# Optimization experiments

Hardware: AMD Instinct MI355X
Metric: run time of the kernel (lower is better)

## Reference

```python
import jax, jax.numpy as jnp
import numpy as np

N, E, G = 50000, 500000, 2048
IN_ATOM, IN_BOND, H, OUT = 128, 16, 256, 2


def setup_inputs() -> dict:
    key = jax.random.key(0)
    ks = iter(jax.random.split(key, 64))
    nrm = lambda shape, s=0.05: jax.random.normal(next(ks), shape, dtype=jnp.float32) * s
    inp = {}
    inp["x"] = nrm((N, IN_ATOM), 1.0)
    inp["edge_attr"] = nrm((E, IN_BOND), 1.0)
    inp["edge_index"] = jax.random.randint(next(ks), (2, E), 0, N)
    inp["batch"] = jnp.sort(jax.random.randint(next(ks), (N,), 0, G))
    dims = [IN_ATOM, H, H]  # input width of each GINE layer
    for i, d in enumerate(dims):
        inp[f"l{i}_We"] = nrm((IN_BOND, d))            # GINEConv edge lin
        inp[f"l{i}_be"] = jnp.zeros((d,), jnp.float32)
        inp[f"l{i}_W1"] = nrm((d, H))                  # mlp Linear 1
        inp[f"l{i}_b1"] = jnp.zeros((H,), jnp.float32)
        inp[f"l{i}_W2"] = nrm((H, H))                  # mlp Linear 2
        inp[f"l{i}_b2"] = jnp.zeros((H,), jnp.float32)
        inp[f"l{i}_eps"] = jnp.zeros((1,), jnp.float32)  # train_eps scalar
    # Bayesian head: weight = mu + exp(log_sigma) * noise
    inp["h1_wmu"] = nrm((H, H)); inp["h1_wls"] = jnp.full((H, H), -3.0, jnp.float32)
    inp["h1_bmu"] = jnp.zeros((H,), jnp.float32); inp["h1_bls"] = jnp.full((H,), -3.0, jnp.float32)
    inp["h2_wmu"] = nrm((H, OUT)); inp["h2_wls"] = jnp.full((H, OUT), -3.0, jnp.float32)
    inp["h2_bmu"] = jnp.zeros((OUT,), jnp.float32); inp["h2_bls"] = jnp.full((OUT,), -3.0, jnp.float32)
    inp["eps_w1"] = nrm((H, H), 1.0); inp["eps_b1"] = nrm((H,), 1.0)
    inp["eps_w2"] = nrm((H, OUT), 1.0); inp["eps_b2"] = nrm((OUT,), 1.0)
    return inp


def _gine_layer(h, src, dst, edge_attr, We, be, W1, b1, W2, b2, eps):
    e = edge_attr @ We + be                       # [E, d] edge projection
    m = jax.nn.relu(h[src] + e)                   # messages from source nodes
    agg = jax.ops.segment_sum(m, dst, num_segments=N)
    z = (1.0 + eps[0]) * h + agg
    z = jax.nn.relu(z @ W1 + b1) @ W2 + b2        # GINE mlp
    return jax.nn.relu(z)                          # backbone activation


def reference(x, edge_attr,
              l0_We, l0_be, l0_W1, l0_b1, l0_W2, l0_b2, l0_eps,
              l1_We, l1_be, l1_W1, l1_b1, l1_W2, l1_b2, l1_eps,
              l2_We, l2_be, l2_W1, l2_b1, l2_W2, l2_b2, l2_eps,
              h1_wmu, h1_wls, h1_bmu, h1_bls,
              h2_wmu, h2_wls, h2_bmu, h2_bls,
              eps_w1, eps_b1, eps_w2, eps_b2,
              edge_index, batch):
    src, dst = edge_index[0], edge_index[1]
    h = x
    layers = [
        (l0_We, l0_be, l0_W1, l0_b1, l0_W2, l0_b2, l0_eps),
        (l1_We, l1_be, l1_W1, l1_b1, l1_W2, l1_b2, l1_eps),
        (l2_We, l2_be, l2_W1, l2_b1, l2_W2, l2_b2, l2_eps),
    ]
    for (We, be, W1, b1, W2, b2, eps) in layers:
        h = _gine_layer(h, src, dst, edge_attr, We, be, W1, b1, W2, b2, eps)
    hg = jax.ops.segment_sum(h, batch, num_segments=G)  # global_add_pool -> [G, H]
    # Bayesian head (dropout is identity at eval)
    w1 = h1_wmu + jnp.exp(h1_wls) * eps_w1
    b1 = h1_bmu + jnp.exp(h1_bls) * eps_b1
    h1 = jax.nn.silu(hg @ w1 + b1)
    w2 = h2_wmu + jnp.exp(h2_wls) * eps_w2
    b2 = h2_bmu + jnp.exp(h2_bls) * eps_b2
    return h1 @ w2 + b2  # [G, OUT]
```

## Files before the change

### kernel.cpp

```cpp
#include <hip/hip_runtime.h>
#include <hip/hip_bf16.h>
#include <math.h>


#define THREADS 256

typedef __attribute__((ext_vector_type(8))) short bf16x8;
typedef __attribute__((ext_vector_type(4))) float f32x4;

__device__ __forceinline__ unsigned short f2bf(float x) {
    __hip_bfloat16 h = __float2bfloat16(x);
    return __builtin_bit_cast(unsigned short, h);
}
__device__ __forceinline__ float bflo(unsigned u) {
    return __builtin_bit_cast(float, u << 16);
}
__device__ __forceinline__ float bfhi(unsigned u) {
    return __builtin_bit_cast(float, u & 0xffff0000u);
}
__device__ __forceinline__ float bf2f(unsigned short u) {
    return __builtin_bit_cast(float, (unsigned)u << 16);
}
__device__ __forceinline__ unsigned pk(float a, float b) {
    return (unsigned)f2bf(a) | ((unsigned)f2bf(b) << 16);
}

__global__ __launch_bounds__(THREADS) void hist_kernel(
    const int* __restrict__ ei, int* __restrict__ deg, int E)
{
    int e = blockIdx.x * THREADS + threadIdx.x;
    if (e < E) atomicAdd(&deg[ei[E + e]], 1);
}

__global__ __launch_bounds__(1024) void scan_kernel(
    int* __restrict__ deg, int* __restrict__ rowptr, int n)
{
    __shared__ int wsum[16];
    __shared__ int carry_s;
    const int t    = threadIdx.x;
    const int lane = t & 63, wv = t >> 6;
    if (t == 0) carry_s = 0;
    __syncthreads();
    for (int base = 0; base < n; base += 4096) {
        int i = base + t * 4;
        int4 v = make_int4(0, 0, 0, 0);
        if (i + 3 < n) {
            v = *(const int4*)(deg + i);
            *(int4*)(deg + i) = make_int4(0, 0, 0, 0);
        } else if (i < n) {
            v.x = deg[i];                    deg[i] = 0;
            if (i + 1 < n) { v.y = deg[i+1]; deg[i+1] = 0; }
            if (i + 2 < n) { v.z = deg[i+2]; deg[i+2] = 0; }
        }
        int p1 = v.x + v.y, p2 = p1 + v.z, tot = p2 + v.w;
        int incl = tot;
#pragma unroll
        for (int off = 1; off < 64; off <<= 1) {
            int u = __shfl_up(incl, off, 64);
            if (lane >= off) incl += u;
        }
        if (lane == 63) wsum[wv] = incl;
        __syncthreads();
        if (wv == 0) {
            int s = (lane < 16) ? wsum[lane] : 0;
#pragma unroll
            for (int off = 1; off < 16; off <<= 1) {
                int u = __shfl_up(s, off, 64);
                if (lane >= off) s += u;
            }
            if (lane < 16) wsum[lane] = s;
        }
        __syncthreads();
        int waveoff = (wv == 0) ? 0 : wsum[wv - 1];
        int tbase   = carry_s + waveoff + incl - tot;
        if (i     < n) rowptr[i + 1] = tbase + v.x;
        if (i + 1 < n) rowptr[i + 2] = tbase + p1;
        if (i + 2 < n) rowptr[i + 3] = tbase + p2;
        if (i + 3 < n) rowptr[i + 4] = tbase + tot;
        __syncthreads();
        if (t == 1023) carry_s = carry_s + wsum[15];
        __syncthreads();
    }
    if (t == 0) rowptr[0] = 0;
}

__global__ __launch_bounds__(THREADS) void fill_kernel(
    const int* __restrict__ ei, const int* __restrict__ rowptr,
    int* __restrict__ cursor, int* __restrict__ csr_src,
    int* __restrict__ csr_dst, const float* __restrict__ edge_attr,
    unsigned short* __restrict__ ea16, int E)
{
    int e = blockIdx.x * THREADS + threadIdx.x;
    if (e >= E) return;
    int s = ei[e], d = ei[E + e];
    int pos  = atomicAdd(&cursor[d], 1);
    int slot = rowptr[d] + pos;
    csr_src[slot] = s;
    csr_dst[slot] = d;
    const float4* a = (const float4*)(edge_attr + (size_t)e * 16);
    float4 a0 = a[0], a1 = a[1], a2 = a[2], a3 = a[3];
    uint4* dst = (uint4*)(ea16 + (size_t)slot * 16);
    dst[0] = make_uint4(pk(a0.x, a0.y), pk(a0.z, a0.w), pk(a1.x, a1.y), pk(a1.z, a1.w));
    dst[1] = make_uint4(pk(a2.x, a2.y), pk(a2.z, a2.w), pk(a3.x, a3.y), pk(a3.z, a3.w));
}

__global__ __launch_bounds__(THREADS) void xprep_kernel(
    const float* __restrict__ x, unsigned short* __restrict__ xbf, int n4,
    uint4* __restrict__ aggz, int nAgg4,
    float4* __restrict__ hgz, int nHg4)
{
    int i = blockIdx.x * THREADS + threadIdx.x;
    if (i < n4) {
        float4 v = ((const float4*)x)[i];
        uint2 p;
        p.x = pk(v.x, v.y);
        p.y = pk(v.z, v.w);
        ((uint2*)xbf)[i] = p;
    }
    if (i < nAgg4) aggz[i] = make_uint4(0, 0, 0, 0);
    if (i < nHg4)  hgz[i]  = make_float4(0.f, 0.f, 0.f, 0.f);
}

struct PrepArgs {
    const float* W[6]; unsigned short* Wt[6]; int K[6];
    const float* mu; const float* ls; const float* eps; float* w1buf;
    const float* We[3]; unsigned short* Wp[3]; int D[3];
};
__global__ __launch_bounds__(THREADS) void prep_kernel(PrepArgs a)
{
    __shared__ float tile[32][33];
    const int z = blockIdx.z;
    const int t = threadIdx.x;

    if (z < 6) {
        const int K = a.K[z];
        const int kb = blockIdx.x * 32;
        if (kb >= K) return;
        const float* W = a.W[z];
        unsigned short* Wt = a.Wt[z];
        const int nb = blockIdx.y * 32;
        const int tx = t & 31, ty = t >> 5;
#pragma unroll
        for (int i = ty; i < 32; i += 8)
            tile[i][tx] = W[(size_t)(kb + i) * 256 + nb + tx];
        __syncthreads();
#pragma unroll
        for (int i = ty; i < 32; i += 8)
            Wt[(size_t)(nb + i) * K + kb + tx] = f2bf(tile[tx][i]);
    } else if (z == 6) {
        int blk = blockIdx.x + blockIdx.y * 8;
#pragma unroll
        for (int c = 0; c < 4; c++) {
            int i = blk * THREADS + t + c * 16384;
            a.w1buf[i] = a.mu[i] + expf(a.ls[i]) * a.eps[i];
        }
    } else {
        int l = blockIdx.x + blockIdx.y * 8;
        if (l >= 3) return;
        int D = a.D[l];
        if (t >= D) return;
        const float* We = a.We[l];
        unsigned short* Wp = a.Wp[l];
#pragma unroll
        for (int k = 0; k < 16; k++) Wp[t * 32 + k] = f2bf(We[k * D + t]);
#pragma unroll
        for (int k = 16; k < 32; k++) Wp[t * 32 + k] = 0;
    }
}

template<int D>
__global__ __launch_bounds__(THREADS) void edge_agg_kernel(
    const unsigned short* __restrict__ hbf,
    const unsigned short* __restrict__ ea16,
    const int* __restrict__ csr_src,
    const int* __restrict__ csr_dst,
    const unsigned short* __restrict__ Wtp,
    const float* __restrict__ be,
    unsigned short* __restrict__ agg,
    int E)
{
    constexpr int EPB = (D == 128) ? 64 : 32;
    constexpr int LDF = D + 8;
    __shared__ unsigned short msg[EPB * LDF];
    __shared__ int src_s[EPB];
    __shared__ int dst_x[EPB + 2];

    const int t    = threadIdx.x;
    const int e0   = blockIdx.x * EPB;
    const int lane = t & 63, wid = t >> 6;
    const int l15  = lane & 15, lgr = lane >> 4;

    for (int i = t; i < EPB; i += THREADS) {
        int e = e0 + i;
        src_s[i] = (e < E) ? csr_src[e] : 0;
    }
    for (int i = t; i < EPB + 2; i += THREADS) {
        int e = e0 + i - 1;
        dst_x[i] = (e < 0) ? -2 : ((e < E) ? csr_dst[e] : -1);
    }

    const int fb = (D == 128) ? (wid & 1) * 64 : wid * 64;
    const int eb = (D == 128) ? (wid >> 1) * 32 : 0;

    bf16x8 af[4];
#pragma unroll
    for (int mf = 0; mf < 4; mf++)
        af[mf] = *(const bf16x8*)(Wtp + (unsigned)(fb + mf * 16 + l15) * 32 + lgr * 8);

    f32x4 acc[4][2];
#pragma unroll
    for (int mf = 0; mf < 4; mf++) {
        int fpos = fb + mf * 16 + lgr * 4;
        float4 bv4 = *(const float4*)(be + fpos);
        f32x4 binit = (f32x4){bv4.x, bv4.y, bv4.z, bv4.w};
        acc[mf][0] = binit;
        acc[mf][1] = binit;
    }

#pragma unroll
    for (int nf = 0; nf < 2; nf++) {
        int er = e0 + eb + nf * 16 + l15;
        bf16x8 bv = (bf16x8){0, 0, 0, 0, 0, 0, 0, 0};
        if (lgr < 2 && er < E)
            bv = *(const bf16x8*)(ea16 + (size_t)er * 16 + lgr * 8);
#pragma unroll
        for (int mf = 0; mf < 4; mf++)
            acc[mf][nf] = __builtin_amdgcn_mfma_f32_16x16x32_bf16(
                af[mf], bv, acc[mf][nf], 0, 0, 0);
    }

#pragma unroll
    for (int nf = 0; nf < 2; nf++) {
        int edge = eb + nf * 16 + l15;
#pragma unroll
        for (int mf = 0; mf < 4; mf++) {
            int fpos = fb + mf * 16 + lgr * 4;
            f32x4 v = acc[mf][nf];
            uint2 p;
            p.x = pk(v[0], v[1]);
            p.y = pk(v[2], v[3]);
            *(uint2*)(&msg[edge * LDF + fpos]) = p;
        }
    }
    __syncthreads();

    constexpr int LPF = D / 2;
    const int f2   = (t & (LPF - 1)) * 2;
    const int win  = t / LPF;
    const int base = win * 16;

    unsigned hv[16], pv[16];
#pragma unroll
    for (int i = 0; i < 16; i++) {
        unsigned off = (unsigned)src_s[base + i] * D + f2;
        hv[i] = *(const unsigned*)(hbf + off);
        pv[i] = *(const unsigned*)(&msg[(base + i) * LDF + f2]);
    }

    float a0 = 0.f, a1 = 0.f;
    int  cur = dst_x[base + 1];
    bool rs  = (dst_x[base] != cur);

#pragma unroll
    for (int i = 0; i < 16; ++i) {
        int el = base + i;
        int d  = dst_x[el + 1];
        if (d != cur) {
            if (cur >= 0) {
                unsigned short* ap = agg + ((unsigned)cur * D + f2);
                unsigned v32 = pk(a0, a1);
                if (rs) {
                    *(unsigned*)ap = v32;
                } else {
                    asm volatile("global_atomic_pk_add_bf16 %0, %1, off"
                                 :: "v"(ap), "v"(v32) : "memory");
                }
            }
            a0 = 0.f; a1 = 0.f; rs = true; cur = d;
        }
        a0 += fmaxf(bflo(hv[i]) + bflo(pv[i]), 0.f);
        a1 += fmaxf(bfhi(hv[i]) + bfhi(pv[i]), 0.f);
    }
    if (cur >= 0) {
        bool re = (dst_x[base + 17] != cur);
        unsigned short* ap = agg + ((unsigned)cur * D + f2);
        unsigned v32 = pk(a0, a1);
        if (rs && re) {
            *(unsigned*)ap = v32;
        } else {
            asm volatile("global_atomic_pk_add_bf16 %0, %1, off"
                         :: "v"(ap), "v"(v32) : "memory");
        }
    }
}

template<int KIN, bool ZERO>
__global__ __launch_bounds__(THREADS) void fused_mlp_kernel(
    const unsigned short* __restrict__ hin,
    const unsigned short* __restrict__ agg,
    const unsigned short* __restrict__ Wt1,
    const float* __restrict__ b1,
    const unsigned short* __restrict__ Wt2,
    const float* __restrict__ b2,
    const float* __restrict__ epsp,
    unsigned short* __restrict__ out,
    uint4* __restrict__ aggz,
    int nrows)
{
    constexpr int LDT = 264;
    __shared__ short Buf[64 * LDT];

    const int t    = threadIdx.x;
    const int lane = t & 63;
    const int wid  = t >> 6;
    const int l15  = lane & 15, lgr = lane >> 4;
    const int r0   = blockIdx.x * 64;

    const float scale = 1.0f + epsp[0];

    constexpr int RU = KIN / 8;
#pragma unroll
    for (int c = 0; c < (64 * RU) / THREADS; c++) {
        int idx = t + c * THREADS;
        int r   = idx / RU;
        int kq  = idx % RU;
        int row = r0 + r;
        uint4 o = make_uint4(0, 0, 0, 0);
        if (row < nrows) {
            size_t g = (size_t)row * KIN + kq * 8;
            uint4 hv = *(const uint4*)(hin + g);
            uint4 av = *(const uint4*)(agg + g);
            o.x = pk(scale * bflo(hv.x) + bflo(av.x),
                     scale * bfhi(hv.x) + bfhi(av.x));
            o.y = pk(scale * bflo(hv.y) + bflo(av.y),
                     scale * bfhi(hv.y) + bfhi(av.y));
            o.z = pk(scale * bflo(hv.z) + bflo(av.z),
                     scale * bfhi(hv.z) + bfhi(av.z));
            o.w = pk(scale * bflo(hv.w) + bflo(av.w),
                     scale * bfhi(hv.w) + bfhi(av.w));
        }
        *(uint4*)(&Buf[r * LDT + kq * 8]) = o;
    }
    __syncthreads();

    if (ZERO) {
        const unsigned aggTot8 = (unsigned)nrows * 32;
        const uint4 zz = make_uint4(0, 0, 0, 0);
        if (KIN == 256) {
            unsigned b8 = (unsigned)blockIdx.x * 2048;
#pragma unroll
            for (int c = 0; c < 8; c++) {
                unsigned idx = b8 + t + c * THREADS;
                if (idx < aggTot8) aggz[idx] = zz;
            }
        } else {
            unsigned own  = (unsigned)blockIdx.x * 1024;
            unsigned tail = ((unsigned)gridDim.x + (unsigned)blockIdx.x) * 1024;
#pragma unroll
            for (int c = 0; c < 4; c++) {
                unsigned i1 = own + t + c * THREADS;
                if (i1 < aggTot8) aggz[i1] = zz;
                unsigned i2 = tail + t + c * THREADS;
                if (i2 < aggTot8) aggz[i2] = zz;
            }
        }
    }

    f32x4 acc[4][4];
#pragma unroll
    for (int nf = 0; nf < 4; nf++) {
        float bv = b1[wid * 64 + nf * 16 + l15];
#pragma unroll
        for (int mf = 0; mf < 4; mf++)
            acc[mf][nf] = (f32x4){bv, bv, bv, bv};
    }

#pragma unroll
    for (int k0 = 0; k0 < KIN; k0 += 64) {
#pragma unroll
        for (int ks = 0; ks < 2; ks++) {
            bf16x8 afr[4], bfr[4];
#pragma unroll
            for (int nf = 0; nf < 4; nf++)
                bfr[nf] = *(const bf16x8*)(Wt1 +
                    (size_t)(wid * 64 + nf * 16 + l15) * KIN + k0 + ks * 32 + lgr * 8);
#pragma unroll
            for (int mf = 0; mf < 4; mf++)
                afr[mf] = *(const bf16x8*)(&Buf[(mf * 16 + l15) * LDT + k0 + ks * 32 + lgr * 8]);
#pragma unroll
            for (int mf = 0; mf < 4; mf++)
#pragma unroll
                for (int nf = 0; nf < 4; nf++)
                    acc[mf][nf] = __builtin_amdgcn_mfma_f32_16x16x32_bf16(
                        afr[mf], bfr[nf], acc[mf][nf], 0, 0, 0);
        }
    }
    __syncthreads();

#pragma unroll
    for (int nf = 0; nf < 4; nf++) {
        int col = wid * 64 + nf * 16 + l15;
#pragma unroll
        for (int mf = 0; mf < 4; mf++) {
            f32x4 v = acc[mf][nf];
#pragma unroll
            for (int r = 0; r < 4; r++) {
                int row = mf * 16 + lgr * 4 + r;
                Buf[row * LDT + col] = (short)f2bf(fmaxf(v[r], 0.f));
            }
        }
    }
#pragma unroll
    for (int nf = 0; nf < 4; nf++) {
        float bv = b2[wid * 64 + nf * 16 + l15];
#pragma unroll
        for (int mf = 0; mf < 4; mf++)
            acc[mf][nf] = (f32x4){bv, bv, bv, bv};
    }
    __syncthreads();

#pragma unroll
    for (int k0 = 0; k0 < 256; k0 += 64) {
#pragma unroll
        for (int ks = 0; ks < 2; ks++) {
            bf16x8 afr[4], bfr[4];
#pragma unroll
            for (int nf = 0; nf < 4; nf++)
                bfr[nf] = *(const bf16x8*)(Wt2 +
                    (size_t)(wid * 64 + nf * 16 + l15) * 256 + k0 + ks * 32 + lgr * 8);
#pragma unroll
            for (int mf = 0; mf < 4; mf++)
                afr[mf] = *(const bf16x8*)(&Buf[(mf * 16 + l15) * LDT + k0 + ks * 32 + lgr * 8]);
#pragma unroll
            for (int mf = 0; mf < 4; mf++)
#pragma unroll
                for (int nf = 0; nf < 4; nf++)
                    acc[mf][nf] = __builtin_amdgcn_mfma_f32_16x16x32_bf16(
                        afr[mf], bfr[nf], acc[mf][nf], 0, 0, 0);
        }
    }

#pragma unroll
    for (int nf = 0; nf < 4; nf++) {
        int col = wid * 64 + nf * 16 + l15;
#pragma unroll
        for (int mf = 0; mf < 4; mf++) {
            f32x4 v = acc[mf][nf];
#pragma unroll
            for (int r = 0; r < 4; r++) {
                int row = r0 + mf * 16 + lgr * 4 + r;
                if (row < nrows)
                    out[(size_t)row * 256 + col] = f2bf(fmaxf(v[r], 0.f));
            }
        }
    }
}

__global__ __launch_bounds__(THREADS) void pool_kernel(
    const unsigned short* __restrict__ hbf,
    const int*   __restrict__ batch,
    float*       __restrict__ hg,
    int nnodes)
{
    constexpr int CH = 64;
    __shared__ int b_s[CH];
    const int t  = threadIdx.x;
    const int v0 = blockIdx.x * CH;
    int cnt = nnodes - v0;
    if (cnt > CH) cnt = CH;
    if (cnt <= 0) return;
    if (t < cnt) b_s[t] = batch[v0 + t];
    __syncthreads();

    int curb  = b_s[0];
    float acc = 0.f;
    for (int v = 0; v < cnt; v++) {
        int b = b_s[v];
        if (b != curb) {
            atomicAdd(&hg[(size_t)curb * 256 + t], acc);
            acc = 0.f; curb = b;
        }
        acc += bf2f(hbf[(size_t)(v0 + v) * 256 + t]);
    }
    atomicAdd(&hg[(size_t)curb * 256 + t], acc);
}

__global__ __launch_bounds__(THREADS) void head_kernel(
    const float* __restrict__ hg,
    const float* __restrict__ w1,
    const float* __restrict__ h1_bmu, const float* __restrict__ h1_bls,
    const float* __restrict__ eps_b1,
    const float* __restrict__ h2_wmu, const float* __restrict__ h2_wls,
    const float* __restrict__ eps_w2,
    const float* __restrict__ h2_bmu, const float* __restrict__ h2_bls,
    const float* __restrict__ eps_b2,
    float* __restrict__ out)
{
    __shared__ float x_s[256];
    __shared__ float red[256];
    const int t = threadIdx.x;
    const int g = blockIdx.x;

    x_s[t] = hg[(size_t)g * 256 + t];
    __syncthreads();

    float acc = h1_bmu[t] + expf(h1_bls[t]) * eps_b1[t];
    for (int kk = 0; kk < 256; kk++) acc += x_s[kk] * w1[kk * 256 + t];
    float h1v = acc / (1.f + expf(-acc));

    float w2a = h2_wmu[t * 2 + 0] + expf(h2_wls[t * 2 + 0]) * eps_w2[t * 2 + 0];
    float w2b = h2_wmu[t * 2 + 1] + expf(h2_wls[t * 2 + 1]) * eps_w2[t * 2 + 1];

    red[t] = h1v * w2a;
    __syncthreads();
    for (int s = 128; s > 0; s >>= 1) {
        if (t < s) red[t] += red[t + s];
        __syncthreads();
    }
    if (t == 0) out[(size_t)g * 2 + 0] = red[0] + h2_bmu[0] + expf(h2_bls[0]) * eps_b2[0];
    __syncthreads();

    red[t] = h1v * w2b;
    __syncthreads();
    for (int s = 128; s > 0; s >>= 1) {
        if (t < s) red[t] += red[t + s];
        __syncthreads();
    }
    if (t == 0) out[(size_t)g * 2 + 1] = red[0] + h2_bmu[1] + expf(h2_bls[1]) * eps_b2[1];
}

extern "C" void kernel_launch(void* const* d_in, const int* in_sizes, int n_in,
                              void* d_out, int out_size, void* d_ws, size_t ws_size,
                              hipStream_t stream)
{
    const float* x         = (const float*)d_in[0];
    const float* edge_attr = (const float*)d_in[1];
    const int*   ei        = (const int*)d_in[2];
    const int*   batch     = (const int*)d_in[3];

    const float* We[3]  = { (const float*)d_in[4],  (const float*)d_in[11], (const float*)d_in[18] };
    const float* be[3]  = { (const float*)d_in[5],  (const float*)d_in[12], (const float*)d_in[19] };
    const float* W1[3]  = { (const float*)d_in[6],  (const float*)d_in[13], (const float*)d_in[20] };
    const float* b1[3]  = { (const float*)d_in[7],  (const float*)d_in[14], (const float*)d_in[21] };
    const float* W2[3]  = { (const float*)d_in[8],  (const float*)d_in[15], (const float*)d_in[22] };
    const float* b2[3]  = { (const float*)d_in[9],  (const float*)d_in[16], (const float*)d_in[23] };
    const float* epsl[3]= { (const float*)d_in[10], (const float*)d_in[17], (const float*)d_in[24] };

    const float* h1_wmu = (const float*)d_in[25];
    const float* h1_wls = (const float*)d_in[26];
    const float* h1_bmu = (const float*)d_in[27];
    const float* h1_bls = (const float*)d_in[28];
    const float* h2_wmu = (const float*)d_in[29];
    const float* h2_wls = (const float*)d_in[30];
    const float* h2_bmu = (const float*)d_in[31];
    const float* h2_bls = (const float*)d_in[32];
    const float* eps_w1 = (const float*)d_in[33];
    const float* eps_b1 = (const float*)d_in[34];
    const float* eps_w2 = (const float*)d_in[35];
    const float* eps_b2 = (const float*)d_in[36];

    const int N = in_sizes[0] / 128;
    const int E = in_sizes[1] / 16;
    const int G = out_size / 2;

    uintptr_t p = (uintptr_t)d_ws;
    auto carve = [&](size_t bytes) -> void* {
        void* r = (void*)p;
        p = (p + bytes + 255) & ~(uintptr_t)255;
        return r;
    };
    float* hg      = (float*)carve((size_t)G * 256 * 4);
    float* w1buf   = (float*)carve(256 * 256 * 4);
    int*   rowptr  = (int*)carve((size_t)(N + 1) * 4);
    int*   cursor  = (int*)carve((size_t)N * 4);
    int*   csr_src = (int*)carve((size_t)E * 4);
    int*   csr_dst = (int*)carve((size_t)E * 4);
    unsigned short* aggbf = (unsigned short*)carve(((size_t)N * 256 + 16384) * 2);
    unsigned short* ea16  = (unsigned short*)carve((size_t)E * 16 * 2);
    unsigned short* hbf   = (unsigned short*)carve((size_t)N * 256 * 2);
    unsigned short* xbf   = (unsigned short*)carve((size_t)N * 128 * 2);
    unsigned short* wep[3];
    wep[0] = (unsigned short*)carve(128 * 32 * 2);
    wep[1] = (unsigned short*)carve(256 * 32 * 2);
    wep[2] = (unsigned short*)carve(256 * 32 * 2);
    unsigned short* wt1[3], *wt2[3];
    wt1[0] = (unsigned short*)carve(256 * 128 * 2);
    for (int l = 0; l < 3; l++) {
        if (l) wt1[l] = (unsigned short*)carve(256 * 256 * 2);
        wt2[l] = (unsigned short*)carve(256 * 256 * 2);
    }

    const int eblocks     = (E + THREADS - 1) / THREADS;
    const int pool_blocks = (N + 63) / 64;
    const int mlp_blocks  = (N + 63) / 64;

    float* out = (float*)d_out;

    hipMemsetAsync(cursor, 0, (size_t)N * sizeof(int), stream);
    hist_kernel<<<eblocks, THREADS, 0, stream>>>(ei, cursor, E);
    scan_kernel<<<1, 1024, 0, stream>>>(cursor, rowptr, N);
    fill_kernel<<<eblocks, THREADS, 0, stream>>>(
        ei, rowptr, cursor, csr_src, csr_dst, edge_attr, ea16, E);
    xprep_kernel<<<(N * 32 + THREADS - 1) / THREADS, THREADS, 0, stream>>>(
        x, xbf, N * 32, (uint4*)aggbf, N * 32, (float4*)hg, G * 64);

    PrepArgs pa;
    pa.W[0] = W1[0]; pa.Wt[0] = wt1[0]; pa.K[0] = 128;
    pa.W[1] = W2[0]; pa.Wt[1] = wt2[0]; pa.K[1] = 256;
    pa.W[2] = W1[1]; pa.Wt[2] = wt1[1]; pa.K[2] = 256;
    pa.W[3] = W2[1]; pa.Wt[3] = wt2[1]; pa.K[3] = 256;
    pa.W[4] = W1[2]; pa.Wt[4] = wt1[2]; pa.K[4] = 256;
    pa.W[5] = W2[2]; pa.Wt[5] = wt2[2]; pa.K[5] = 256;
    pa.mu = h1_wmu; pa.ls = h1_wls; pa.eps = eps_w1; pa.w1buf = w1buf;
    for (int l = 0; l < 3; l++) { pa.We[l] = We[l]; pa.Wp[l] = wep[l]; }
    pa.D[0] = 128; pa.D[1] = 256; pa.D[2] = 256;
    prep_kernel<<<dim3(8, 8, 8), THREADS, 0, stream>>>(pa);

    edge_agg_kernel<128><<<(E + 63) / 64, THREADS, 0, stream>>>(
        xbf, ea16, csr_src, csr_dst, wep[0], be[0], aggbf, E);
    fused_mlp_kernel<128, true><<<mlp_blocks, THREADS, 0, stream>>>(
        xbf, aggbf, wt1[0], b1[0], wt2[0], b2[0], epsl[0], hbf, (uint4*)aggbf, N);

    edge_agg_kernel<256><<<(E + 31) / 32, THREADS, 0, stream>>>(
        hbf, ea16, csr_src, csr_dst, wep[1], be[1], aggbf, E);
    fused_mlp_kernel<256, true><<<mlp_blocks, THREADS, 0, stream>>>(
        hbf, aggbf, wt1[1], b1[1], wt2[1], b2[1], epsl[1], hbf, (uint4*)aggbf, N);

    edge_agg_kernel<256><<<(E + 31) / 32, THREADS, 0, stream>>>(
        hbf, ea16, csr_src, csr_dst, wep[2], be[2], aggbf, E);
    fused_mlp_kernel<256, false><<<mlp_blocks, THREADS, 0, stream>>>(
        hbf, aggbf, wt1[2], b1[2], wt2[2], b2[2], epsl[2], hbf, (uint4*)aggbf, N);

    pool_kernel<<<pool_blocks, THREADS, 0, stream>>>(hbf, batch, hg, N);

    head_kernel<<<G, THREADS, 0, stream>>>(
        hg, w1buf, h1_bmu, h1_bls, eps_b1,
        h2_wmu, h2_wls, eps_w2, h2_bmu, h2_bls, eps_b2, out);
}
```

Baseline: 413.9 us.

## Widen edge aggregation per block and fuse global pooling into last MLP

Edge aggregation now covers twice as many edges per block and has each thread handle four features with 64-bit loads instead of two with 32-bit loads, which halves the block count and the per-edge index and bookkeeping overhead. The separate pool kernel is removed: the final fused MLP kernel writes its ReLU output to shared memory and does the segmented sum into hg directly. This skips writing the final node features to global memory and reading them back. In exchange it adds shared-memory traffic and two extra block barriers, the atomic path now issues two packed atomics per run, and shared-memory use per block rises in the edge kernel.

```diff
diff --git a/kernel.cpp b/kernel.cpp
--- a/kernel.cpp
+++ b/kernel.cpp
@@ -179,7 +179,7 @@
     unsigned short* __restrict__ agg,
     int E)
 {
-    constexpr int EPB = (D == 128) ? 64 : 32;
+    constexpr int EPB = (D == 128) ? 128 : 64;
     constexpr int LDF = D + 8;
     __shared__ unsigned short msg[EPB * LDF];
     __shared__ int src_s[EPB];
@@ -200,25 +200,25 @@
     }
 
     const int fb = (D == 128) ? (wid & 1) * 64 : wid * 64;
-    const int eb = (D == 128) ? (wid >> 1) * 32 : 0;
+    const int eb = (D == 128) ? (wid >> 1) * 64 : 0;
 
     bf16x8 af[4];
 #pragma unroll
     for (int mf = 0; mf < 4; mf++)
         af[mf] = *(const bf16x8*)(Wtp + (unsigned)(fb + mf * 16 + l15) * 32 + lgr * 8);
 
-    f32x4 acc[4][2];
+    f32x4 acc[4][4];
 #pragma unroll
     for (int mf = 0; mf < 4; mf++) {
         int fpos = fb + mf * 16 + lgr * 4;
         float4 bv4 = *(const float4*)(be + fpos);
         f32x4 binit = (f32x4){bv4.x, bv4.y, bv4.z, bv4.w};
-        acc[mf][0] = binit;
-        acc[mf][1] = binit;
-    }
-
-#pragma unroll
-    for (int nf = 0; nf < 2; nf++) {
+#pragma unroll
+        for (int nf = 0; nf < 4; nf++) acc[mf][nf] = binit;
+    }
+
+#pragma unroll
+    for (int nf = 0; nf < 4; nf++) {
         int er = e0 + eb + nf * 16 + l15;
         bf16x8 bv = (bf16x8){0, 0, 0, 0, 0, 0, 0, 0};
         if (lgr < 2 && er < E)
@@ -230,7 +230,7 @@
     }
 
 #pragma unroll
-    for (int nf = 0; nf < 2; nf++) {
+    for (int nf = 0; nf < 4; nf++) {
         int edge = eb + nf * 16 + l15;
 #pragma unroll
         for (int mf = 0; mf < 4; mf++) {
@@ -244,57 +244,63 @@
     }
     __syncthreads();
 
-    constexpr int LPF = D / 2;
-    const int f2   = (t & (LPF - 1)) * 2;
+    constexpr int LPF = D / 4;
+    const int f4   = (t & (LPF - 1)) * 4;
     const int win  = t / LPF;
     const int base = win * 16;
 
-    unsigned hv[16], pv[16];
+    uint2 hv[16], pv[16];
 #pragma unroll
     for (int i = 0; i < 16; i++) {
-        unsigned off = (unsigned)src_s[base + i] * D + f2;
-        hv[i] = *(const unsigned*)(hbf + off);
-        pv[i] = *(const unsigned*)(&msg[(base + i) * LDF + f2]);
-    }
-
-    float a0 = 0.f, a1 = 0.f;
+        unsigned off = (unsigned)src_s[base + i] * D + f4;
+        hv[i] = *(const uint2*)(hbf + off);
+        pv[i] = *(const uint2*)(&msg[(base + i) * LDF + f4]);
+    }
+
+    float a0 = 0.f, a1 = 0.f, a2 = 0.f, a3 = 0.f;
     int  cur = dst_x[base + 1];
     bool rs  = (dst_x[base] != cur);
 
 #pragma unroll
     for (int i = 0; i < 16; ++i) {
-        int el = base + i;
-        int d  = dst_x[el + 1];
+        int d = dst_x[base + i + 1];
         if (d != cur) {
             if (cur >= 0) {
-                unsigned short* ap = agg + ((unsigned)cur * D + f2);
-                unsigned v32 = pk(a0, a1);
+                unsigned short* ap = agg + ((unsigned)cur * D + f4);
+                unsigned p0 = pk(a0, a1), p1 = pk(a2, a3);
                 if (rs) {
-                    *(unsigned*)ap = v32;
+                    *(uint2*)ap = make_uint2(p0, p1);
                 } else {
                     asm volatile("global_atomic_pk_add_bf16 %0, %1, off"
-                                 :: "v"(ap), "v"(v32) : "memory");
+                                 :: "v"(ap), "v"(p0) : "memory");
+                    asm volatile("global_atomic_pk_add_bf16 %0, %1, off"
+                                 :: "v"(ap + 2), "v"(p1) : "memory");
                 }
             }
-            a0 = 0.f; a1 = 0.f; rs = true; cur = d;
-        }
-        a0 += fmaxf(bflo(hv[i]) + bflo(pv[i]), 0.f);
-        a1 += fmaxf(bfhi(hv[i]) + bfhi(pv[i]), 0.f);
+            a0 = 0.f; a1 = 0.f; a2 = 0.f; a3 = 0.f;
+            rs = true; cur = d;
+        }
+        a0 += fmaxf(bflo(hv[i].x) + bflo(pv[i].x), 0.f);
+        a1 += fmaxf(bfhi(hv[i].x) + bfhi(pv[i].x), 0.f);
+        a2 += fmaxf(bflo(hv[i].y) + bflo(pv[i].y), 0.f);
+        a3 += fmaxf(bfhi(hv[i].y) + bfhi(pv[i].y), 0.f);
     }
     if (cur >= 0) {
         bool re = (dst_x[base + 17] != cur);
-        unsigned short* ap = agg + ((unsigned)cur * D + f2);
-        unsigned v32 = pk(a0, a1);
+        unsigned short* ap = agg + ((unsigned)cur * D + f4);
+        unsigned p0 = pk(a0, a1), p1 = pk(a2, a3);
         if (rs && re) {
-            *(unsigned*)ap = v32;
+            *(uint2*)ap = make_uint2(p0, p1);
         } else {
             asm volatile("global_atomic_pk_add_bf16 %0, %1, off"
-                         :: "v"(ap), "v"(v32) : "memory");
-        }
-    }
-}
-
-template<int KIN, bool ZERO>
+                         :: "v"(ap), "v"(p0) : "memory");
+            asm volatile("global_atomic_pk_add_bf16 %0, %1, off"
+                         :: "v"(ap + 2), "v"(p1) : "memory");
+        }
+    }
+}
+
+template<int KIN, bool ZERO, bool POOL>
 __global__ __launch_bounds__(THREADS) void fused_mlp_kernel(
     const unsigned short* __restrict__ hin,
     const unsigned short* __restrict__ agg,
@@ -305,10 +311,13 @@
     const float* __restrict__ epsp,
     unsigned short* __restrict__ out,
     uint4* __restrict__ aggz,
+    const int* __restrict__ batch,
+    float* __restrict__ hg,
     int nrows)
 {
     constexpr int LDT = 264;
     __shared__ short Buf[64 * LDT];
+    __shared__ int bat[64];
 
     const int t    = threadIdx.x;
     const int lane = t & 63;
@@ -341,6 +350,10 @@
         }
         *(uint4*)(&Buf[r * LDT + kq * 8]) = o;
     }
+    if (POOL && t < 64) {
+        int row = r0 + t;
+        bat[t] = (row < nrows) ? batch[row] : -1;
+    }
     __syncthreads();
 
     if (ZERO) {
@@ -440,49 +453,50 @@
         }
     }
 
-#pragma unroll
-    for (int nf = 0; nf < 4; nf++) {
-        int col = wid * 64 + nf * 16 + l15;
-#pragma unroll
-        for (int mf = 0; mf < 4; mf++) {
-            f32x4 v = acc[mf][nf];
-#pragma unroll
-            for (int r = 0; r < 4; r++) {
-                int row = r0 + mf * 16 + lgr * 4 + r;
-                if (row < nrows)
-                    out[(size_t)row * 256 + col] = f2bf(fmaxf(v[r], 0.f));
-            }
-        }
-    }
-}
-
-__global__ __launch_bounds__(THREADS) void pool_kernel(
-    const unsigned short* __restrict__ hbf,
-    const int*   __restrict__ batch,
-    float*       __restrict__ hg,
-    int nnodes)
-{
-    constexpr int CH = 64;
-    __shared__ int b_s[CH];
-    const int t  = threadIdx.x;
-    const int v0 = blockIdx.x * CH;
-    int cnt = nnodes - v0;
-    if (cnt > CH) cnt = CH;
-    if (cnt <= 0) return;
-    if (t < cnt) b_s[t] = batch[v0 + t];
-    __syncthreads();
-
-    int curb  = b_s[0];
-    float acc = 0.f;
-    for (int v = 0; v < cnt; v++) {
-        int b = b_s[v];
-        if (b != curb) {
-            atomicAdd(&hg[(size_t)curb * 256 + t], acc);
-            acc = 0.f; curb = b;
-        }
-        acc += bf2f(hbf[(size_t)(v0 + v) * 256 + t]);
-    }
-    atomicAdd(&hg[(size_t)curb * 256 + t], acc);
+    if (!POOL) {
+#pragma unroll
+        for (int nf = 0; nf < 4; nf++) {
+            int col = wid * 64 + nf * 16 + l15;
+#pragma unroll
+            for (int mf = 0; mf < 4; mf++) {
+                f32x4 v = acc[mf][nf];
+#pragma unroll
+                for (int r = 0; r < 4; r++) {
+                    int row = r0 + mf * 16 + lgr * 4 + r;
+                    if (row < nrows)
+                        out[(size_t)row * 256 + col] = f2bf(fmaxf(v[r], 0.f));
+                }
+            }
+        }
+    } else {
+        __syncthreads();
+#pragma unroll
+        for (int nf = 0; nf < 4; nf++) {
+            int col = wid * 64 + nf * 16 + l15;
+#pragma unroll
+            for (int mf = 0; mf < 4; mf++) {
+                f32x4 v = acc[mf][nf];
+#pragma unroll
+                for (int r = 0; r < 4; r++) {
+                    int row = mf * 16 + lgr * 4 + r;
+                    Buf[row * LDT + col] = (short)f2bf(fmaxf(v[r], 0.f));
+                }
+            }
+        }
+        __syncthreads();
+
+        float a = 0.f;
+        int cur = bat[0];
+        for (int r = 0; r < 64; ++r) {
+            int b = bat[r];
+            if (b != cur) {
+                if (cur >= 0) atomicAdd(&hg[(size_t)cur * 256 + t], a);
+                a = 0.f; cur = b;
+            }
+            a += bf2f((unsigned short)Buf[r * LDT + t]);
+        }
+        if (cur >= 0) atomicAdd(&hg[(size_t)cur * 256 + t], a);
+    }
 }
 
 __global__ __launch_bounds__(THREADS) void head_kernel(
@@ -590,9 +604,8 @@
         wt2[l] = (unsigned short*)carve(256 * 256 * 2);
     }
 
-    const int eblocks     = (E + THREADS - 1) / THREADS;
-    const int pool_blocks = (N + 63) / 64;
-    const int mlp_blocks  = (N + 63) / 64;
+    const int eblocks    = (E + THREADS - 1) / THREADS;
+    const int mlp_blocks = (N + 63) / 64;
 
     float* out = (float*)d_out;
 
@@ -616,22 +629,23 @@
     pa.D[0] = 128; pa.D[1] = 256; pa.D[2] = 256;
     prep_kernel<<<dim3(8, 8, 8), THREADS, 0, stream>>>(pa);
 
-    edge_agg_kernel<128><<<(E + 63) / 64, THREADS, 0, stream>>>(
+    edge_agg_kernel<128><<<(E + 127) / 128, THREADS, 0, stream>>>(
         xbf, ea16, csr_src, csr_dst, wep[0], be[0], aggbf, E);
-    fused_mlp_kernel<128, true><<<mlp_blocks, THREADS, 0, stream>>>(
-        xbf, aggbf, wt1[0], b1[0], wt2[0], b2[0], epsl[0], hbf, (uint4*)aggbf, N);
-
-    edge_agg_kernel<256><<<(E + 31) / 32, THREADS, 0, stream>>>(
+    fused_mlp_kernel<128, true, false><<<mlp_blocks, THREADS, 0, stream>>>(
+        xbf, aggbf, wt1[0], b1[0], wt2[0], b2[0], epsl[0], hbf, (uint4*)aggbf,
+        nullptr, nullptr, N);
+
+    edge_agg_kernel<256><<<(E + 63) / 64, THREADS, 0, stream>>>(
         hbf, ea16, csr_src, csr_dst, wep[1], be[1], aggbf, E);
-    fused_mlp_kernel<256, true><<<mlp_blocks, THREADS, 0, stream>>>(
-        hbf, aggbf, wt1[1], b1[1], wt2[1], b2[1], epsl[1], hbf, (uint4*)aggbf, N);
-
-    edge_agg_kernel<256><<<(E + 31) / 32, THREADS, 0, stream>>>(
+    fused_mlp_kernel<256, true, false><<<mlp_blocks, THREADS, 0, stream>>>(
+        hbf, aggbf, wt1[1], b1[1], wt2[1], b2[1], epsl[1], hbf, (uint4*)aggbf,
+        nullptr, nullptr, N);
+
+    edge_agg_kernel<256><<<(E + 63) / 64, THREADS, 0, stream>>>(
         hbf, ea16, csr_src, csr_dst, wep[2], be[2], aggbf, E);
-    fused_mlp_kernel<256, false><<<mlp_blocks, THREADS, 0, stream>>>(
-        hbf, aggbf, wt1[2], b1[2], wt2[2], b2[2], epsl[2], hbf, (uint4*)aggbf, N);
-
-    pool_kernel<<<pool_blocks, THREADS, 0, stream>>>(hbf, batch, hg, N);
+    fused_mlp_kernel<256, false, true><<<mlp_blocks, THREADS, 0, stream>>>(
+        hbf, aggbf, wt1[2], b1[2], wt2[2], b2[2], epsl[2], hbf, (uint4*)aggbf,
+        batch, hg, N);
 
     head_kernel<<<G, THREADS, 0, stream>>>(
         hg, w1buf, h1_bmu, h1_bls, eps_b1,
```

After: 425.6 us. 2.8% more time.
